# Performance work log

Measured on AMD Instinct MI355X. Metric: run time of the kernel, lower is better.

The kernel has to match this reference:

```python
import math
import jax, jax.numpy as jnp
import numpy as np

N_HEADS = 16


def setup_inputs() -> dict:
    key = jax.random.key(0)
    k1, k2 = jax.random.split(key)
    N, H, C, T = 2, N_HEADS, 64, 2048
    qkv = jax.random.normal(k1, (N, H * 3 * C, T), dtype=jnp.float32)
    mask = jax.random.randint(k2, (N, 1, T), 0, 2).astype(bool) | (jnp.arange(T)[None, None, :] < T // 2)
    return {"qkv": qkv, "mask": mask}


def reference(qkv, mask):
    bs, width, length = qkv.shape
    ch = width // (3 * N_HEADS)
    qkv_r = qkv.reshape(bs * N_HEADS, 3 * ch, length)
    q, k, v = qkv_r[:, :ch], qkv_r[:, ch:2 * ch], qkv_r[:, 2 * ch:]
    scale = 1.0 / math.sqrt(math.sqrt(ch))
    # [bH, T, T] scores in float32 (matches weight.float())
    weight = jnp.einsum('bct,bcs->bts', q * scale, k * scale).astype(jnp.float32)
    inv = ~mask[:, 0, :]                                   # [N, T] True = pad
    m = inv[:, None, :] | inv[:, :, None]                  # [N, T, T]
    m = jnp.broadcast_to(m[:, None], (bs, N_HEADS, length, length)).reshape(-1, length, length)
    weight = jnp.where(m, jnp.finfo(weight.dtype).min, weight)
    weight = jax.nn.softmax(weight, axis=-1)
    a = jnp.einsum('bts,bcs->bct', weight, v)              # [bH, C, T]
    return a.reshape(bs, -1, length)
```

## Files before the change

### kernel.cpp

```cpp
#include <hip/hip_runtime.h>
#include <hip/hip_bf16.h>
#include <stdint.h>

namespace {

constexpr int T_LEN = 2048;
constexpr int NROWS = 192;
constexpr int QBLK  = 64;
constexpr int NBH   = 32;
constexpr int KT_STRIDE = 72;
constexpr int TILE_ELEMS = 64 * KT_STRIDE;

typedef float f32x4 __attribute__((ext_vector_type(4)));
typedef short bf16x8 __attribute__((ext_vector_type(8)));
typedef short bf16x4 __attribute__((ext_vector_type(4)));

__device__ __forceinline__ unsigned short f2bf(float f) {
  union { float f; unsigned u; } v; v.f = f;
  unsigned r = v.u + 0x7fffu + ((v.u >> 16) & 1u);
  return (unsigned short)(r >> 16);
}
__device__ __forceinline__ unsigned pack2(float a, float b) {
  return (unsigned)f2bf(a) | ((unsigned)f2bf(b) << 16);
}
__device__ __forceinline__ float fast_exp2(float x) {
#if __has_builtin(__builtin_amdgcn_exp2f)
  return __builtin_amdgcn_exp2f(x);
#else
  return exp2f(x);
#endif
}
__device__ __forceinline__ f32x4 mfma_16x16x16_bf16(bf16x4 a, bf16x4 b, f32x4 c) {
#if __has_builtin(__builtin_amdgcn_mfma_f32_16x16x16bf16_1k)
  return __builtin_amdgcn_mfma_f32_16x16x16bf16_1k(a, b, c, 0, 0, 0);
#else
  asm("v_mfma_f32_16x16x16_bf16 %0, %1, %2, %0" : "+v"(c) : "v"(a), "v"(b));
  return c;
#endif
}

}

__global__ void nm_kernel(const unsigned char* __restrict__ raw,
                          unsigned char* __restrict__ outm, int n) {
  int stride = (raw[1] != 0) ? 1 : ((raw[4] != 0) ? 4 : 8);
  int i = blockIdx.x * blockDim.x + threadIdx.x;
  if (i < n) outm[i] = (raw[(size_t)i * stride] != 0) ? 1 : 0;
}


__global__ __launch_bounds__(256) void tq3_kernel(const float* __restrict__ qkv,
                                                  short* __restrict__ qtg,
                                                  short* __restrict__ ktg) {
  __shared__ float tile[64][65];
  const int t = threadIdx.x;
  const int which = blockIdx.z;
  const int bh = blockIdx.y;
  const int bx = blockIdx.x;
  const int s0 = bx * 64;
  const float* src = qkv + (size_t)bh * NROWS * T_LEN + (size_t)which * 64 * T_LEN;
  const int c = t >> 2;
  #pragma unroll
  for (int p = 0; p < 4; ++p) {
    int col = (t & 3) * 4 + p * 16;
    float4 v = *(const float4*)&src[(size_t)c * T_LEN + s0 + col];
    tile[c][col] = v.x; tile[c][col + 1] = v.y;
    tile[c][col + 2] = v.z; tile[c][col + 3] = v.w;
  }
  __syncthreads();
  const float scale = which ? 1.0f : 0.18033688011112042f;
  const int s = t & 63;
  #pragma unroll
  for (int p = 0; p < 2; ++p) {
    int jc = (t >> 6) * 2 + p;
    bf16x4 o0, o1;
    #pragma unroll
    for (int i = 0; i < 4; ++i) {
      o0[i] = (short)f2bf(tile[jc * 8 + i][s] * scale);
      o1[i] = (short)f2bf(tile[jc * 8 + 4 + i][s] * scale);
    }
    short* d = which
      ? (ktg + (size_t)(bh * 32 + bx) * TILE_ELEMS + s * KT_STRIDE + jc * 8)
      : (qtg + (size_t)bh * T_LEN * 64 + (size_t)(s0 + s) * 64 + jc * 8);
    *(bf16x4*)d = o0;
    *(bf16x4*)(d + 4) = o1;
  }
}

__global__ __launch_bounds__(256) void cv3_kernel(const float* __restrict__ qkv,
                                                  short* __restrict__ vtg) {
  int cid = blockIdx.x * 256 + threadIdx.x;
  int bh = cid >> 14;
  int rem = cid & 16383;
  int c = rem >> 8;
  int cg = rem & 255;
  int grp = cg >> 3, jin = cg & 7;
  const float* src = qkv + (size_t)bh * NROWS * T_LEN + (size_t)(128 + c) * T_LEN + cg * 8;
  float4 a = *(const float4*)src;
  float4 b = *(const float4*)(src + 4);
  bf16x4 o0, o1;
  o0[0] = (short)f2bf(a.x); o0[1] = (short)f2bf(a.y);
  o0[2] = (short)f2bf(a.z); o0[3] = (short)f2bf(a.w);
  o1[0] = (short)f2bf(b.x); o1[1] = (short)f2bf(b.y);
  o1[2] = (short)f2bf(b.z); o1[3] = (short)f2bf(b.w);
  short* d = vtg + (size_t)(bh * 32 + grp) * TILE_ELEMS + c * KT_STRIDE + jin * 8;
  *(bf16x4*)d = o0;
  *(bf16x4*)(d + 4) = o1;
}


__global__ __launch_bounds__(256) void attn5_kernel(const short* __restrict__ qtg,
                                                    const short* __restrict__ ktg,
                                                    const short* __restrict__ vtg,
                                                    const unsigned char* __restrict__ maskn,
                                                    float* __restrict__ out) {
  __shared__ __align__(16) short Kt[2][TILE_ELEMS];
  __shared__ __align__(16) short Vs[2][TILE_ELEMS];
  __shared__ __align__(16) unsigned char Ms[T_LEN];

  const int tid  = threadIdx.x;
  const int lane = tid & 63;
  const int wv   = tid >> 6;
  const int l15  = lane & 15;
  const int g    = lane >> 4;

  int id = blockIdx.x;
  id = (id & 7) * 128 + (id >> 3);
  const int bh = id >> 5;
  const int t0 = (id & 31) * QBLK;
  const int nb = bh >> 4;

  ((uint2*)Ms)[tid] = ((const uint2*)(maskn + (size_t)nb * T_LEN))[tid];

  const int t_lane = t0 + wv * 16 + l15;
  const short* Qrow = qtg + (size_t)bh * T_LEN * 64 + (size_t)t_lane * 64;
  const bf16x8 qf0 = *(const bf16x8*)(Qrow + g * 8);
  const bf16x8 qf1 = *(const bf16x8*)(Qrow + 32 + g * 8);

  const bf16x8* __restrict__ kbase = (const bf16x8*)(ktg + (size_t)bh * 32 * TILE_ELEMS);
  const bf16x8* __restrict__ vbase = (const bf16x8*)(vtg + (size_t)bh * 32 * TILE_ELEMS);

  {
    const bf16x8* ks = kbase;
    const bf16x8* vs = vbase;
    bf16x8 k0 = ks[tid], k1 = ks[tid + 256];
    bf16x8 v0 = vs[tid], v1 = vs[tid + 256];
    ((bf16x8*)Kt[0])[tid]       = k0;
    ((bf16x8*)Kt[0])[tid + 256] = k1;
    ((bf16x8*)Vs[0])[tid]       = v0;
    ((bf16x8*)Vs[0])[tid + 256] = v1;
    if (tid < 64) {
      ((bf16x8*)Kt[0])[tid + 512] = ks[tid + 512];
      ((bf16x8*)Vs[0])[tid + 512] = vs[tid + 512];
    }
  }
  __syncthreads();
  const bool invt = (Ms[t_lane] == 0);

  f32x4 acc[4];
  #pragma unroll
  for (int i = 0; i < 4; ++i) acc[i] = (f32x4){0.f, 0.f, 0.f, 0.f};
  float l_part = 0.0f;

  int cur = 0;
  for (int sb = 0; sb < T_LEN / 64; ++sb) {
    bf16x8 k0, k1, k2, v0, v1, v2;
    const bool more = (sb + 1 < T_LEN / 64);
    if (more) {
      const bf16x8* ks = kbase + (size_t)(sb + 1) * (TILE_ELEMS / 8);
      const bf16x8* vs = vbase + (size_t)(sb + 1) * (TILE_ELEMS / 8);
      k0 = ks[tid]; k1 = ks[tid + 256];
      v0 = vs[tid]; v1 = vs[tid + 256];
      if (tid < 64) { k2 = ks[tid + 512]; v2 = vs[tid + 512]; }
    }

    const short* Ktc = Kt[cur];
    const short* Vsc = Vs[cur];
    const int s0 = sb * 64;
    #pragma unroll
    for (int st = 0; st < 4; ++st) {
      const int srow = st * 16 + l15;
      bf16x8 kf0 = *(const bf16x8*)&Ktc[srow * KT_STRIDE + g * 8];
      bf16x8 kf1 = *(const bf16x8*)&Ktc[srow * KT_STRIDE + 32 + g * 8];
      f32x4 S = (f32x4){0.f, 0.f, 0.f, 0.f};
      S = __builtin_amdgcn_mfma_f32_16x16x32_bf16(kf0, qf0, S, 0, 0, 0);
      S = __builtin_amdgcn_mfma_f32_16x16x32_bf16(kf1, qf1, S, 0, 0, 0);

      const unsigned m4 = *(const unsigned*)&Ms[s0 + st * 16 + g * 4];
      float p0, p1, p2, p3;
      {
        float x0 = ((m4 & 0x000000ffu) ? S[0] : -1.0e30f);
        float x1 = ((m4 & 0x0000ff00u) ? S[1] : -1.0e30f);
        float x2 = ((m4 & 0x00ff0000u) ? S[2] : -1.0e30f);
        float x3 = ((m4 & 0xff000000u) ? S[3] : -1.0e30f);
        p0 = fast_exp2(invt ? 0.0f : x0);
        p1 = fast_exp2(invt ? 0.0f : x1);
        p2 = fast_exp2(invt ? 0.0f : x2);
        p3 = fast_exp2(invt ? 0.0f : x3);
      }
      l_part += (p0 + p1) + (p2 + p3);

      union { bf16x4 v; __hip_bfloat162 h[2]; } pf;
      pf.h[0] = __float22bfloat162_rn(float2{p0, p1});
      pf.h[1] = __float22bfloat162_rn(float2{p2, p3});

      #pragma unroll
      for (int cb = 0; cb < 4; ++cb) {
        bf16x4 vf = *(const bf16x4*)&Vsc[(cb * 16 + l15) * KT_STRIDE + st * 16 + g * 4];
        acc[cb] = mfma_16x16x16_bf16(vf, pf.v, acc[cb]);
      }
    }

    if (more) {
      short* Ktn = Kt[cur ^ 1];
      short* Vsn = Vs[cur ^ 1];
      ((bf16x8*)Ktn)[tid]       = k0;
      ((bf16x8*)Ktn)[tid + 256] = k1;
      ((bf16x8*)Vsn)[tid]       = v0;
      ((bf16x8*)Vsn)[tid + 256] = v1;
      if (tid < 64) {
        ((bf16x8*)Ktn)[tid + 512] = k2;
        ((bf16x8*)Vsn)[tid + 512] = v2;
      }
    }
    __syncthreads();
    cur ^= 1;
  }

  l_part += __shfl_xor(l_part, 16, 64);
  l_part += __shfl_xor(l_part, 32, 64);
  const float il = 1.0f / l_part;
  const size_t out_base = (size_t)bh * 64 * T_LEN;
  #pragma unroll
  for (int cb = 0; cb < 4; ++cb) {
    #pragma unroll
    for (int r = 0; r < 4; ++r) {
      int c = cb * 16 + g * 4 + r;
      out[out_base + (size_t)c * T_LEN + t_lane] = acc[cb][r] * il;
    }
  }
}


__global__ __launch_bounds__(256) void attn_fb_kernel(const float* __restrict__ qkv,
                                                      const unsigned char* __restrict__ maskn,
                                                      float* __restrict__ out) {
  __shared__ __align__(16) short Kt[QBLK * KT_STRIDE];
  __shared__ __align__(16) short Vs[64 * KT_STRIDE];
  __shared__ __align__(16) unsigned char Ms[T_LEN];

  const int tid  = threadIdx.x;
  const int lane = tid & 63;
  const int wv   = tid >> 6;
  const int l15  = lane & 15;
  const int g    = lane >> 4;

  const int bh = blockIdx.y;
  const int nb = bh >> 4;
  const int t0 = blockIdx.x * QBLK;

  const float* __restrict__ Qg = qkv + (size_t)bh * NROWS * T_LEN;
  const float* __restrict__ Kg = Qg + (size_t)64 * T_LEN;
  const float* __restrict__ Vg = Qg + (size_t)128 * T_LEN;

  {
    const uint2* src = (const uint2*)(maskn + (size_t)nb * T_LEN);
    ((uint2*)Ms)[tid] = src[tid];
  }
  {
    const int c2 = (tid >> 6) * 2;
    const int s  = tid & 63;
    #pragma unroll
    for (int p = 0; p < 8; ++p) {
      int c = p * 8 + c2;
      float f0 = Qg[(size_t)c * T_LEN + t0 + s] * 0.125f;
      float f1 = Qg[(size_t)(c + 1) * T_LEN + t0 + s] * 0.125f;
      *(unsigned*)&Kt[s * KT_STRIDE + c] = pack2(f0, f1);
    }
  }
  __syncthreads();

  bf16x8 qf0 = *(const bf16x8*)&Kt[(wv * 16 + l15) * KT_STRIDE + g * 8];
  bf16x8 qf1 = *(const bf16x8*)&Kt[(wv * 16 + l15) * KT_STRIDE + 32 + g * 8];
  const int t_lane = t0 + wv * 16 + l15;
  const bool invt = (Ms[t_lane] == 0);

  f32x4 acc[4];
  #pragma unroll
  for (int i = 0; i < 4; ++i) acc[i] = (f32x4){0.f, 0.f, 0.f, 0.f};
  float m_run = -3.0e38f;
  float l_run = 0.0f;

  for (int sb = 0; sb < T_LEN / 64; ++sb) {
    const int s0 = sb * 64;
    __syncthreads();
    {
      const int c2 = (tid >> 6) * 2;
      const int s  = tid & 63;
      #pragma unroll
      for (int p = 0; p < 8; ++p) {
        int c = p * 8 + c2;
        float f0 = Kg[(size_t)c * T_LEN + s0 + s];
        float f1 = Kg[(size_t)(c + 1) * T_LEN + s0 + s];
        *(unsigned*)&Kt[s * KT_STRIDE + c] = pack2(f0, f1);
      }
    }
    {
      const int cv = (tid >> 5);
      const int s2 = tid & 31;
      #pragma unroll
      for (int p = 0; p < 8; ++p) {
        int c = p * 8 + cv;
        float2 f = *(const float2*)&Vg[(size_t)c * T_LEN + s0 + 2 * s2];
        *(unsigned*)&Vs[c * KT_STRIDE + 2 * s2] = pack2(f.x, f.y);
      }
    }
    __syncthreads();

    #pragma unroll
    for (int st = 0; st < 4; ++st) {
      const int srow = st * 16 + l15;
      bf16x8 kf0 = *(const bf16x8*)&Kt[srow * KT_STRIDE + g * 8];
      bf16x8 kf1 = *(const bf16x8*)&Kt[srow * KT_STRIDE + 32 + g * 8];
      f32x4 S = (f32x4){0.f, 0.f, 0.f, 0.f};
      S = __builtin_amdgcn_mfma_f32_16x16x32_bf16(kf0, qf0, S, 0, 0, 0);
      S = __builtin_amdgcn_mfma_f32_16x16x32_bf16(kf1, qf1, S, 0, 0, 0);

      const unsigned m4 = *(const unsigned*)&Ms[s0 + st * 16 + g * 4];
      float vals[4];
      #pragma unroll
      for (int r = 0; r < 4; ++r) {
        float x = ((m4 >> (8 * r)) & 0xffu) ? S[r] : -1.0e30f;
        vals[r] = invt ? 0.0f : x;
      }
      float pm = fmaxf(fmaxf(vals[0], vals[1]), fmaxf(vals[2], vals[3]));
      pm = fmaxf(pm, __shfl_xor(pm, 16, 64));
      pm = fmaxf(pm, __shfl_xor(pm, 32, 64));
      const float newm = fmaxf(m_run, pm);
      const float alpha = fast_exp2((m_run - newm) * 1.44269504f);
      float p0 = fast_exp2((vals[0] - newm) * 1.44269504f);
      float p1 = fast_exp2((vals[1] - newm) * 1.44269504f);
      float p2 = fast_exp2((vals[2] - newm) * 1.44269504f);
      float p3 = fast_exp2((vals[3] - newm) * 1.44269504f);
      float ps = (p0 + p1) + (p2 + p3);
      ps += __shfl_xor(ps, 16, 64);
      ps += __shfl_xor(ps, 32, 64);
      l_run = l_run * alpha + ps;
      m_run = newm;
      if (__any(alpha < 1.0f)) {
        #pragma unroll
        for (int cb = 0; cb < 4; ++cb)
          #pragma unroll
          for (int r = 0; r < 4; ++r) acc[cb][r] *= alpha;
      }
      bf16x4 pf;
      pf[0] = (short)f2bf(p0); pf[1] = (short)f2bf(p1);
      pf[2] = (short)f2bf(p2); pf[3] = (short)f2bf(p3);
      #pragma unroll
      for (int cb = 0; cb < 4; ++cb) {
        bf16x4 vf = *(const bf16x4*)&Vs[(cb * 16 + l15) * KT_STRIDE + st * 16 + g * 4];
        acc[cb] = mfma_16x16x16_bf16(vf, pf, acc[cb]);
      }
    }
  }

  const float il = 1.0f / l_run;
  const size_t out_base = (size_t)bh * 64 * T_LEN;
  #pragma unroll
  for (int cb = 0; cb < 4; ++cb) {
    #pragma unroll
    for (int r = 0; r < 4; ++r) {
      int c = cb * 16 + g * 4 + r;
      out[out_base + (size_t)c * T_LEN + t_lane] = acc[cb][r] * il;
    }
  }
}


extern "C" void kernel_launch(void* const* d_in, const int* in_sizes, int n_in,
                              void* d_out, int out_size, void* d_ws, size_t ws_size,
                              hipStream_t stream) {
  (void)n_in; (void)out_size;
  const float* qkv = (const float*)d_in[0];
  const unsigned char* mraw = (const unsigned char*)d_in[1];
  float* out = (float*)d_out;
  const int mask_elems = in_sizes[1];

  const size_t QSZ = (size_t)NBH * T_LEN * 64 * sizeof(short);
  const size_t TSZ = (size_t)NBH * 32 * TILE_ELEMS * sizeof(short);
  const size_t need = QSZ + 2 * TSZ + (size_t)mask_elems;
  if (ws_size >= need) {
    short* qtg = (short*)d_ws;
    short* ktg = (short*)((char*)d_ws + QSZ);
    short* vtg = (short*)((char*)d_ws + QSZ + TSZ);
    unsigned char* maskn = (unsigned char*)d_ws + QSZ + 2 * TSZ;
    nm_kernel<<<(mask_elems + 255) / 256, 256, 0, stream>>>(mraw, maskn, mask_elems);
    tq3_kernel<<<dim3(T_LEN / 64, NBH, 2), 256, 0, stream>>>(qkv, qtg, ktg);
    cv3_kernel<<<(NBH * 64 * 256) / 256, 256, 0, stream>>>(qkv, vtg);
    attn5_kernel<<<dim3(NBH * 32), 256, 0, stream>>>(qtg, ktg, vtg, maskn, out);
  } else {
    unsigned char* maskn = (unsigned char*)d_ws;
    nm_kernel<<<(mask_elems + 255) / 256, 256, 0, stream>>>(mraw, maskn, mask_elems);
    attn_fb_kernel<<<dim3(T_LEN / QBLK, NBH), 256, 0, stream>>>(qkv, maskn, out);
  }
}
```

Measured before the change: 95.63 us.

## Split key tiles across two wave groups with shared-memory reduction

Doubles the block to 512 threads. Two groups of four waves each process half of the 16-row key sub-tiles of every 64-key tile, and the tile loads are spread over more threads. At the end the second group writes its partial output accumulators and row sums to shared memory, and the first group adds them and writes the output. The aim is more waves in flight per query block to hide MFMA and exp latency. The cost is an extra reduction phase and a larger register/occupancy footprint per block.

```diff
diff --git a/kernel.cpp b/kernel.cpp
--- a/kernel.cpp
+++ b/kernel.cpp
@@ -109,7 +109,7 @@
 }
 
 
-__global__ __launch_bounds__(256) void attn5_kernel(const short* __restrict__ qtg,
+__global__ __launch_bounds__(512) void attn6_kernel(const short* __restrict__ qtg,
                                                     const short* __restrict__ ktg,
                                                     const short* __restrict__ vtg,
                                                     const unsigned char* __restrict__ maskn,
@@ -121,6 +121,8 @@
   const int tid  = threadIdx.x;
   const int lane = tid & 63;
   const int wv   = tid >> 6;
+  const int tw   = wv & 3;
+  const int sh   = wv >> 2;
   const int l15  = lane & 15;
   const int g    = lane >> 4;
 
@@ -130,9 +132,9 @@
   const int t0 = (id & 31) * QBLK;
   const int nb = bh >> 4;
 
-  ((uint2*)Ms)[tid] = ((const uint2*)(maskn + (size_t)nb * T_LEN))[tid];
-
-  const int t_lane = t0 + wv * 16 + l15;
+  if (tid < 256) ((uint2*)Ms)[tid] = ((const uint2*)(maskn + (size_t)nb * T_LEN))[tid];
+
+  const int t_lane = t0 + tw * 16 + l15;
   const short* Qrow = qtg + (size_t)bh * T_LEN * 64 + (size_t)t_lane * 64;
   const bf16x8 qf0 = *(const bf16x8*)(Qrow + g * 8);
   const bf16x8 qf1 = *(const bf16x8*)(Qrow + 32 + g * 8);
@@ -143,12 +145,8 @@
   {
     const bf16x8* ks = kbase;
     const bf16x8* vs = vbase;
-    bf16x8 k0 = ks[tid], k1 = ks[tid + 256];
-    bf16x8 v0 = vs[tid], v1 = vs[tid + 256];
-    ((bf16x8*)Kt[0])[tid]       = k0;
-    ((bf16x8*)Kt[0])[tid + 256] = k1;
-    ((bf16x8*)Vs[0])[tid]       = v0;
-    ((bf16x8*)Vs[0])[tid + 256] = v1;
+    ((bf16x8*)Kt[0])[tid] = ks[tid];
+    ((bf16x8*)Vs[0])[tid] = vs[tid];
     if (tid < 64) {
       ((bf16x8*)Kt[0])[tid + 512] = ks[tid + 512];
       ((bf16x8*)Vs[0])[tid + 512] = vs[tid + 512];
@@ -164,21 +162,21 @@
 
   int cur = 0;
   for (int sb = 0; sb < T_LEN / 64; ++sb) {
-    bf16x8 k0, k1, k2, v0, v1, v2;
+    bf16x8 k0, k1, v0, v1;
     const bool more = (sb + 1 < T_LEN / 64);
     if (more) {
       const bf16x8* ks = kbase + (size_t)(sb + 1) * (TILE_ELEMS / 8);
       const bf16x8* vs = vbase + (size_t)(sb + 1) * (TILE_ELEMS / 8);
-      k0 = ks[tid]; k1 = ks[tid + 256];
-      v0 = vs[tid]; v1 = vs[tid + 256];
-      if (tid < 64) { k2 = ks[tid + 512]; v2 = vs[tid + 512]; }
+      k0 = ks[tid]; v0 = vs[tid];
+      if (tid < 64) { k1 = ks[tid + 512]; v1 = vs[tid + 512]; }
     }
 
     const short* Ktc = Kt[cur];
     const short* Vsc = Vs[cur];
     const int s0 = sb * 64;
     #pragma unroll
-    for (int st = 0; st < 4; ++st) {
+    for (int sti = 0; sti < 2; ++sti) {
+      const int st = sh * 2 + sti;
       const int srow = st * 16 + l15;
       bf16x8 kf0 = *(const bf16x8*)&Ktc[srow * KT_STRIDE + g * 8];
       bf16x8 kf1 = *(const bf16x8*)&Ktc[srow * KT_STRIDE + 32 + g * 8];
@@ -214,29 +212,43 @@
     if (more) {
       short* Ktn = Kt[cur ^ 1];
       short* Vsn = Vs[cur ^ 1];
-      ((bf16x8*)Ktn)[tid]       = k0;
-      ((bf16x8*)Ktn)[tid + 256] = k1;
-      ((bf16x8*)Vsn)[tid]       = v0;
-      ((bf16x8*)Vsn)[tid + 256] = v1;
+      ((bf16x8*)Ktn)[tid] = k0;
+      ((bf16x8*)Vsn)[tid] = v0;
       if (tid < 64) {
-        ((bf16x8*)Ktn)[tid + 512] = k2;
-        ((bf16x8*)Vsn)[tid + 512] = v2;
+        ((bf16x8*)Ktn)[tid + 512] = k1;
+        ((bf16x8*)Vsn)[tid + 512] = v1;
       }
     }
     __syncthreads();
     cur ^= 1;
   }
 
-  l_part += __shfl_xor(l_part, 16, 64);
-  l_part += __shfl_xor(l_part, 32, 64);
-  const float il = 1.0f / l_part;
-  const size_t out_base = (size_t)bh * 64 * T_LEN;
-  #pragma unroll
-  for (int cb = 0; cb < 4; ++cb) {
-    #pragma unroll
-    for (int r = 0; r < 4; ++r) {
-      int c = cb * 16 + g * 4 + r;
-      out[out_base + (size_t)c * T_LEN + t_lane] = acc[cb][r] * il;
+  float* scratch = (float*)Kt;
+  const int trow = tw * 16 + l15;
+  if (wv >= 4) {
+    float* row = scratch + trow * 68;
+    #pragma unroll
+    for (int cb = 0; cb < 4; ++cb) *(f32x4*)&row[cb * 16 + g * 4] = acc[cb];
+    row[64 + g] = l_part;
+  }
+  __syncthreads();
+  if (wv < 4) {
+    const float* row = scratch + trow * 68;
+    #pragma unroll
+    for (int cb = 0; cb < 4; ++cb) acc[cb] += *(const f32x4*)&row[cb * 16 + g * 4];
+    l_part += row[64 + g];
+
+    l_part += __shfl_xor(l_part, 16, 64);
+    l_part += __shfl_xor(l_part, 32, 64);
+    const float il = 1.0f / l_part;
+    const size_t out_base = (size_t)bh * 64 * T_LEN;
+    #pragma unroll
+    for (int cb = 0; cb < 4; ++cb) {
+      #pragma unroll
+      for (int r = 0; r < 4; ++r) {
+        int c = cb * 16 + g * 4 + r;
+        out[out_base + (size_t)c * T_LEN + t_lane] = acc[cb][r] * il;
+      }
     }
   }
 }
@@ -397,7 +409,7 @@
     nm_kernel<<<(mask_elems + 255) / 256, 256, 0, stream>>>(mraw, maskn, mask_elems);
     tq3_kernel<<<dim3(T_LEN / 64, NBH, 2), 256, 0, stream>>>(qkv, qtg, ktg);
     cv3_kernel<<<(NBH * 64 * 256) / 256, 256, 0, stream>>>(qkv, vtg);
-    attn5_kernel<<<dim3(NBH * 32), 256, 0, stream>>>(qtg, ktg, vtg, maskn, out);
+    attn6_kernel<<<dim3(NBH * 32), 512, 0, stream>>>(qtg, ktg, vtg, maskn, out);
   } else {
     unsigned char* maskn = (unsigned char*)d_ws;
     nm_kernel<<<(mask_elems + 255) / 256, 256, 0, stream>>>(mraw, maskn, mask_elems);
```

Result: faster. 91.56 us (-4.3%).

## Split key dimension across waves and reduce partial outputs through shared memory

Applied to the files above, without the earlier changes.

Instead of each wave owning 16 query rows and looping over all 64 keys of a tile, each wave now owns 16 keys of every tile and processes all 64 query rows. Q fragments for all four row groups are held in registers, so each K/V fragment read from LDS is reused four times. The change cuts LDS reads per MFMA. In exchange it raises register pressure (a 4x4 accumulator array) and adds a cross-wave tree reduction of accumulators and row sums through shared memory at the end. The unnormalized exp-sum design without a running max is unchanged.

```diff
diff --git a/kernel.cpp b/kernel.cpp
--- a/kernel.cpp
+++ b/kernel.cpp
@@ -109,13 +109,12 @@
 }
 
 
-__global__ __launch_bounds__(256) void attn5_kernel(const short* __restrict__ qtg,
+__global__ __launch_bounds__(256) void attn7_kernel(const short* __restrict__ qtg,
                                                     const short* __restrict__ ktg,
                                                     const short* __restrict__ vtg,
                                                     const unsigned char* __restrict__ maskn,
                                                     float* __restrict__ out) {
-  __shared__ __align__(16) short Kt[2][TILE_ELEMS];
-  __shared__ __align__(16) short Vs[2][TILE_ELEMS];
+  __shared__ __align__(16) short smem[4 * TILE_ELEMS];
   __shared__ __align__(16) unsigned char Ms[T_LEN];
 
   const int tid  = threadIdx.x;
@@ -132,10 +131,13 @@
 
   ((uint2*)Ms)[tid] = ((const uint2*)(maskn + (size_t)nb * T_LEN))[tid];
 
-  const int t_lane = t0 + wv * 16 + l15;
-  const short* Qrow = qtg + (size_t)bh * T_LEN * 64 + (size_t)t_lane * 64;
-  const bf16x8 qf0 = *(const bf16x8*)(Qrow + g * 8);
-  const bf16x8 qf1 = *(const bf16x8*)(Qrow + 32 + g * 8);
+  bf16x8 qf0[4], qf1[4];
+  #pragma unroll
+  for (int tw = 0; tw < 4; ++tw) {
+    const short* Qrow = qtg + (size_t)bh * T_LEN * 64 + (size_t)(t0 + tw * 16 + l15) * 64;
+    qf0[tw] = *(const bf16x8*)(Qrow + g * 8);
+    qf1[tw] = *(const bf16x8*)(Qrow + 32 + g * 8);
+  }
 
   const bf16x8* __restrict__ kbase = (const bf16x8*)(ktg + (size_t)bh * 32 * TILE_ELEMS);
   const bf16x8* __restrict__ vbase = (const bf16x8*)(vtg + (size_t)bh * 32 * TILE_ELEMS);
@@ -143,24 +145,29 @@
   {
     const bf16x8* ks = kbase;
     const bf16x8* vs = vbase;
-    bf16x8 k0 = ks[tid], k1 = ks[tid + 256];
-    bf16x8 v0 = vs[tid], v1 = vs[tid + 256];
-    ((bf16x8*)Kt[0])[tid]       = k0;
-    ((bf16x8*)Kt[0])[tid + 256] = k1;
-    ((bf16x8*)Vs[0])[tid]       = v0;
-    ((bf16x8*)Vs[0])[tid + 256] = v1;
+    ((bf16x8*)smem)[tid]       = ks[tid];
+    ((bf16x8*)smem)[tid + 256] = ks[tid + 256];
+    ((bf16x8*)(smem + 2 * TILE_ELEMS))[tid]       = vs[tid];
+    ((bf16x8*)(smem + 2 * TILE_ELEMS))[tid + 256] = vs[tid + 256];
     if (tid < 64) {
-      ((bf16x8*)Kt[0])[tid + 512] = ks[tid + 512];
-      ((bf16x8*)Vs[0])[tid + 512] = vs[tid + 512];
-    }
-  }
-  __syncthreads();
-  const bool invt = (Ms[t_lane] == 0);
-
-  f32x4 acc[4];
-  #pragma unroll
-  for (int i = 0; i < 4; ++i) acc[i] = (f32x4){0.f, 0.f, 0.f, 0.f};
-  float l_part = 0.0f;
+      ((bf16x8*)smem)[tid + 512] = ks[tid + 512];
+      ((bf16x8*)(smem + 2 * TILE_ELEMS))[tid + 512] = vs[tid + 512];
+    }
+  }
+  __syncthreads();
+
+  bool invt[4];
+  #pragma unroll
+  for (int tw = 0; tw < 4; ++tw) invt[tw] = (Ms[t0 + tw * 16 + l15] == 0);
+
+  f32x4 acc[4][4];
+  #pragma unroll
+  for (int i = 0; i < 4; ++i)
+    #pragma unroll
+    for (int j = 0; j < 4; ++j) acc[i][j] = (f32x4){0.f, 0.f, 0.f, 0.f};
+  float l_part[4] = {0.f, 0.f, 0.f, 0.f};
+
+  const int koff = (wv * 16 + l15) * KT_STRIDE;
 
   int cur = 0;
   for (int sb = 0; sb < T_LEN / 64; ++sb) {
@@ -174,46 +181,49 @@
       if (tid < 64) { k2 = ks[tid + 512]; v2 = vs[tid + 512]; }
     }
 
-    const short* Ktc = Kt[cur];
-    const short* Vsc = Vs[cur];
+    const short* Ktc = smem + cur * TILE_ELEMS;
+    const short* Vsc = smem + (2 + cur) * TILE_ELEMS;
     const int s0 = sb * 64;
-    #pragma unroll
-    for (int st = 0; st < 4; ++st) {
-      const int srow = st * 16 + l15;
-      bf16x8 kf0 = *(const bf16x8*)&Ktc[srow * KT_STRIDE + g * 8];
-      bf16x8 kf1 = *(const bf16x8*)&Ktc[srow * KT_STRIDE + 32 + g * 8];
-      f32x4 S = (f32x4){0.f, 0.f, 0.f, 0.f};
-      S = __builtin_amdgcn_mfma_f32_16x16x32_bf16(kf0, qf0, S, 0, 0, 0);
-      S = __builtin_amdgcn_mfma_f32_16x16x32_bf16(kf1, qf1, S, 0, 0, 0);
-
-      const unsigned m4 = *(const unsigned*)&Ms[s0 + st * 16 + g * 4];
-      float p0, p1, p2, p3;
-      {
-        float x0 = ((m4 & 0x000000ffu) ? S[0] : -1.0e30f);
-        float x1 = ((m4 & 0x0000ff00u) ? S[1] : -1.0e30f);
-        float x2 = ((m4 & 0x00ff0000u) ? S[2] : -1.0e30f);
-        float x3 = ((m4 & 0xff000000u) ? S[3] : -1.0e30f);
-        p0 = fast_exp2(invt ? 0.0f : x0);
-        p1 = fast_exp2(invt ? 0.0f : x1);
-        p2 = fast_exp2(invt ? 0.0f : x2);
-        p3 = fast_exp2(invt ? 0.0f : x3);
-      }
-      l_part += (p0 + p1) + (p2 + p3);
-
-      union { bf16x4 v; __hip_bfloat162 h[2]; } pf;
-      pf.h[0] = __float22bfloat162_rn(float2{p0, p1});
-      pf.h[1] = __float22bfloat162_rn(float2{p2, p3});
-
-      #pragma unroll
-      for (int cb = 0; cb < 4; ++cb) {
-        bf16x4 vf = *(const bf16x4*)&Vsc[(cb * 16 + l15) * KT_STRIDE + st * 16 + g * 4];
-        acc[cb] = mfma_16x16x16_bf16(vf, pf.v, acc[cb]);
-      }
+
+    bf16x8 kf0 = *(const bf16x8*)&Ktc[koff + g * 8];
+    bf16x8 kf1 = *(const bf16x8*)&Ktc[koff + 32 + g * 8];
+
+    f32x4 S[4];
+    #pragma unroll
+    for (int tw = 0; tw < 4; ++tw) {
+      S[tw] = (f32x4){0.f, 0.f, 0.f, 0.f};
+      S[tw] = __builtin_amdgcn_mfma_f32_16x16x32_bf16(kf0, qf0[tw], S[tw], 0, 0, 0);
+      S[tw] = __builtin_amdgcn_mfma_f32_16x16x32_bf16(kf1, qf1[tw], S[tw], 0, 0, 0);
+    }
+
+    const unsigned m4 = *(const unsigned*)&Ms[s0 + wv * 16 + g * 4];
+    union { bf16x4 v; __hip_bfloat162 h[2]; } pf[4];
+    #pragma unroll
+    for (int tw = 0; tw < 4; ++tw) {
+      float x0 = ((m4 & 0x000000ffu) ? S[tw][0] : -1.0e30f);
+      float x1 = ((m4 & 0x0000ff00u) ? S[tw][1] : -1.0e30f);
+      float x2 = ((m4 & 0x00ff0000u) ? S[tw][2] : -1.0e30f);
+      float x3 = ((m4 & 0xff000000u) ? S[tw][3] : -1.0e30f);
+      float p0 = fast_exp2(invt[tw] ? 0.0f : x0);
+      float p1 = fast_exp2(invt[tw] ? 0.0f : x1);
+      float p2 = fast_exp2(invt[tw] ? 0.0f : x2);
+      float p3 = fast_exp2(invt[tw] ? 0.0f : x3);
+      l_part[tw] += (p0 + p1) + (p2 + p3);
+      pf[tw].h[0] = __float22bfloat162_rn(float2{p0, p1});
+      pf[tw].h[1] = __float22bfloat162_rn(float2{p2, p3});
+    }
+
+    #pragma unroll
+    for (int cb = 0; cb < 4; ++cb) {
+      bf16x4 vf = *(const bf16x4*)&Vsc[(cb * 16 + l15) * KT_STRIDE + wv * 16 + g * 4];
+      #pragma unroll
+      for (int tw = 0; tw < 4; ++tw)
+        acc[tw][cb] = mfma_16x16x16_bf16(vf, pf[tw].v, acc[tw][cb]);
     }
 
     if (more) {
-      short* Ktn = Kt[cur ^ 1];
-      short* Vsn = Vs[cur ^ 1];
+      short* Ktn = smem + (cur ^ 1) * TILE_ELEMS;
+      short* Vsn = smem + (2 + (cur ^ 1)) * TILE_ELEMS;
       ((bf16x8*)Ktn)[tid]       = k0;
       ((bf16x8*)Ktn)[tid + 256] = k1;
       ((bf16x8*)Vsn)[tid]       = v0;
@@ -227,16 +237,62 @@
     cur ^= 1;
   }
 
-  l_part += __shfl_xor(l_part, 16, 64);
-  l_part += __shfl_xor(l_part, 32, 64);
-  const float il = 1.0f / l_part;
-  const size_t out_base = (size_t)bh * 64 * T_LEN;
-  #pragma unroll
-  for (int cb = 0; cb < 4; ++cb) {
-    #pragma unroll
-    for (int r = 0; r < 4; ++r) {
-      int c = cb * 16 + g * 4 + r;
-      out[out_base + (size_t)c * T_LEN + t_lane] = acc[cb][r] * il;
+  float* scr = (float*)smem;
+  const int lbase = lane * 68;
+  if (wv >= 2) {
+    float* slot = scr + (wv - 2) * 4352 + lbase;
+    #pragma unroll
+    for (int tw = 0; tw < 4; ++tw) {
+      #pragma unroll
+      for (int cb = 0; cb < 4; ++cb) *(f32x4*)&slot[tw * 16 + cb * 4] = acc[tw][cb];
+      slot[64 + tw] = l_part[tw];
+    }
+  }
+  __syncthreads();
+  if (wv < 2) {
+    const float* slot = scr + wv * 4352 + lbase;
+    #pragma unroll
+    for (int tw = 0; tw < 4; ++tw) {
+      #pragma unroll
+      for (int cb = 0; cb < 4; ++cb) acc[tw][cb] += *(const f32x4*)&slot[tw * 16 + cb * 4];
+      l_part[tw] += slot[64 + tw];
+    }
+  }
+  __syncthreads();
+  if (wv == 1) {
+    float* slot = scr + lbase;
+    #pragma unroll
+    for (int tw = 0; tw < 4; ++tw) {
+      #pragma unroll
+      for (int cb = 0; cb < 4; ++cb) *(f32x4*)&slot[tw * 16 + cb * 4] = acc[tw][cb];
+      slot[64 + tw] = l_part[tw];
+    }
+  }
+  __syncthreads();
+  if (wv == 0) {
+    const float* slot = scr + lbase;
+    #pragma unroll
+    for (int tw = 0; tw < 4; ++tw) {
+      #pragma unroll
+      for (int cb = 0; cb < 4; ++cb) acc[tw][cb] += *(const f32x4*)&slot[tw * 16 + cb * 4];
+      l_part[tw] += slot[64 + tw];
+    }
+    const size_t out_base = (size_t)bh * 64 * T_LEN;
+    #pragma unroll
+    for (int tw = 0; tw < 4; ++tw) {
+      float l = l_part[tw];
+      l += __shfl_xor(l, 16, 64);
+      l += __shfl_xor(l, 32, 64);
+      const float il = 1.0f / l;
+      const int t = t0 + tw * 16 + l15;
+      #pragma unroll
+      for (int cb = 0; cb < 4; ++cb) {
+        #pragma unroll
+        for (int r = 0; r < 4; ++r) {
+          int c = cb * 16 + g * 4 + r;
+          out[out_base + (size_t)c * T_LEN + t] = acc[tw][cb][r] * il;
+        }
+      }
     }
   }
 }
@@ -397,7 +453,7 @@
     nm_kernel<<<(mask_elems + 255) / 256, 256, 0, stream>>>(mraw, maskn, mask_elems);
     tq3_kernel<<<dim3(T_LEN / 64, NBH, 2), 256, 0, stream>>>(qkv, qtg, ktg);
     cv3_kernel<<<(NBH * 64 * 256) / 256, 256, 0, stream>>>(qkv, vtg);
-    attn5_kernel<<<dim3(NBH * 32), 256, 0, stream>>>(qtg, ktg, vtg, maskn, out);
+    attn7_kernel<<<dim3(NBH * 32), 256, 0, stream>>>(qtg, ktg, vtg, maskn, out);
   } else {
     unsigned char* maskn = (unsigned char*)d_ws;
     nm_kernel<<<(mask_elems + 255) / 256, 256, 0, stream>>>(mraw, maskn, mask_elems);
```

Measured after the change: 97.71 us. 2.2% more time.
